# Kernel optimization log

Hardware: AMD Instinct MI355X
Metric: run time of the kernel (lower is better)

## Reference

```python
import jax, jax.numpy as jnp
import numpy as np
import math

C = 1024
CH = C // 2


def setup_inputs() -> dict:
    key = jax.random.key(0)
    ks = jax.random.split(key, 8)
    B, Nq, Nk = 8, 2048, 2048
    y = jax.random.normal(ks[0], (B, Nq, C), dtype=jnp.float32)
    x = jax.random.normal(ks[1], (B, Nk, C), dtype=jnp.float32)
    # torch nn.Linear weights are [out, in]; custom normal init per module
    Wq = jax.random.normal(ks[2], (CH, C), dtype=jnp.float32) * math.sqrt(2.0 / CH)
    Wk = jax.random.normal(ks[3], (CH, C), dtype=jnp.float32) * math.sqrt(2.0 / CH)
    Wv = jax.random.normal(ks[4], (C, C), dtype=jnp.float32) * math.sqrt(2.0 / C)
    # biases keep default torch Linear init: U(-1/sqrt(in), 1/sqrt(in))
    b = 1.0 / math.sqrt(C)
    bq = jax.random.uniform(ks[5], (CH,), minval=-b, maxval=b, dtype=jnp.float32)
    bk = jax.random.uniform(ks[6], (CH,), minval=-b, maxval=b, dtype=jnp.float32)
    bv = jax.random.uniform(ks[7], (C,), minval=-b, maxval=b, dtype=jnp.float32)
    return {"y": y, "x": x, "Wq": Wq, "bq": bq, "Wk": Wk, "bk": bk, "Wv": Wv, "bv": bv}


def reference(y, x, Wq, bq, Wk, bk, Wv, bv):
    scale = (C // 2) ** (-0.5)
    q = jnp.einsum('bnc,hc->bnh', y, Wq) + bq          # [B, Nq, C/2]
    k = jnp.einsum('bmc,hc->bmh', x, Wk) + bk          # [B, Nk, C/2]
    v = jnp.einsum('bmc,dc->bmd', x, Wv) + bv          # [B, Nk, C]
    dots = jnp.einsum('bnh,bmh->bnm', q, k) * scale    # [B, Nq, Nk]
    attn = jax.nn.softmax(dots, axis=-2)               # softmax over QUERY dim
    out = jnp.einsum('bnm,bmd->bnd', attn, v)          # [B, Nq, C]
    return out
```

## Files before the change

kernel.cpp:

```cpp
#include <hip/hip_runtime.h>
#include <hip/hip_bf16.h>


using bf16 = __bf16;
typedef __attribute__((ext_vector_type(8))) __bf16 bf16x8;
typedef __attribute__((ext_vector_type(4))) float f32x4;

#define GLB_AS __attribute__((address_space(1)))
#define LDS_AS __attribute__((address_space(3)))

__device__ __forceinline__ void gload_lds16(const void* g, void* l) {
  __builtin_amdgcn_global_load_lds((const GLB_AS uint32_t*)g,
                                   (LDS_AS uint32_t*)l, 16, 0, 0);
}

#define BAR() __builtin_amdgcn_s_barrier()
#define LGK0() asm volatile("s_waitcnt lgkmcnt(0)" ::: "memory")
#define VM4() asm volatile("s_waitcnt vmcnt(4)" ::: "memory")
#define VM0() asm volatile("s_waitcnt vmcnt(0)" ::: "memory")

enum { EPI_BIAS = 0, EPI_EXP = 1, EPI_OUT = 2 };

template <int EPI>
__global__ __launch_bounds__(512, 2) void gemm256(
    const bf16* __restrict__ A, const bf16* __restrict__ Bt,
    void* __restrict__ Cv, const float* __restrict__ bias,
    float* __restrict__ Z, int M, int N, int K, int ldA, int ldB, int ldC,
    long sA, long sB, long sC, float scale) {
  __shared__ __align__(16) bf16 As[3 * 8192];
  __shared__ __align__(16) bf16 Bs[3 * 8192];

  const int bz = blockIdx.z;
  const bf16* Ab = A + (long)bz * sA;
  const bf16* Bb = Bt + (long)bz * sB;

  const int tid = threadIdx.x;
  const int lane = tid & 63;
  const int wave = tid >> 6;
  const int wr = wave >> 2;
  const int wc = wave & 3;
  const int fl = lane & 15;
  const int kg = lane >> 4;
  const long m0 = (long)blockIdx.x * 256;
  const long n0 = (long)blockIdx.y * 256;

  f32x4 acc[8][4] = {};

  const int js = tid ^ ((tid >> 3) & 7);
  const int srow = js >> 2;
  const int scol = (js & 3) * 8;
  const bf16* gAc = Ab + (m0 + srow) * (long)ldA + scol;
  const bf16* gBc = Bb + (n0 + srow) * (long)ldB + scol;
  char* Abase = (char*)As;
  char* Bbase = (char*)Bs;

#define STAGE_A(tt)                                         \
  {                                                         \
    char* _d = Abase + ((tt) % 3) * 16384 + tid * 16;       \
    const bf16* _g = gAc + (long)(tt) * 32;                 \
    gload_lds16(_g, _d);                                    \
    gload_lds16(_g + 128 * (long)ldA, _d + 8192);           \
  }
#define STAGE_B(tt)                                         \
  {                                                         \
    char* _d = Bbase + ((tt) % 3) * 16384 + tid * 16;       \
    const bf16* _g = gBc + (long)(tt) * 32;                 \
    gload_lds16(_g, _d);                                    \
    gload_lds16(_g + 128 * (long)ldB, _d + 8192);           \
  }

  const int swz = (fl >> 1) << 4;
  const int abase = ((wr * 128 + fl) * 64 + kg * 16) ^ swz;
  const int bbase = ((wc * 64 + fl) * 64 + kg * 16) ^ swz;

  const int nt = K >> 5;

  STAGE_A(0) STAGE_B(0) STAGE_A(1) STAGE_B(1)
  VM4();
  BAR();

  for (int t = 0; t < nt; ++t) {
    const char* Asl = Abase + (t % 3) * 16384;
    const char* Bsl = Bbase + (t % 3) * 16384;
    bf16x8 a[8], b0, b1;
#pragma unroll
    for (int mi = 0; mi < 8; mi++)
      a[mi] = *(const bf16x8*)(Asl + abase + mi * 1024);
    b0 = *(const bf16x8*)(Bsl + bbase);
    b1 = *(const bf16x8*)(Bsl + bbase + 1024);
    if (t + 2 < nt) STAGE_A(t + 2);
    BAR();
    LGK0();
    __builtin_amdgcn_s_setprio(1);
#pragma unroll
    for (int mi = 0; mi < 8; mi++) {
      acc[mi][0] = __builtin_amdgcn_mfma_f32_16x16x32_bf16(a[mi], b0, acc[mi][0], 0, 0, 0);
      acc[mi][1] = __builtin_amdgcn_mfma_f32_16x16x32_bf16(a[mi], b1, acc[mi][1], 0, 0, 0);
    }
    __builtin_amdgcn_s_setprio(0);
    BAR();
    b0 = *(const bf16x8*)(Bsl + bbase + 2 * 1024);
    b1 = *(const bf16x8*)(Bsl + bbase + 3 * 1024);
    if (t + 2 < nt) STAGE_B(t + 2);
    BAR();
    LGK0();
    __builtin_amdgcn_s_setprio(1);
#pragma unroll
    for (int mi = 0; mi < 8; mi++) {
      acc[mi][2] = __builtin_amdgcn_mfma_f32_16x16x32_bf16(a[mi], b0, acc[mi][2], 0, 0, 0);
      acc[mi][3] = __builtin_amdgcn_mfma_f32_16x16x32_bf16(a[mi], b1, acc[mi][3], 0, 0, 0);
    }
    __builtin_amdgcn_s_setprio(0);
    if (t + 2 < nt) { VM4(); } else { VM0(); }
    BAR();
  }
#undef STAGE_A
#undef STAGE_B

  if constexpr (EPI == EPI_BIAS) {
    bf16* Cb = (bf16*)Cv + (long)bz * sC;
#pragma unroll
    for (int j = 0; j < 4; j++) {
      const long cc = n0 + wc * 64 + j * 16 + fl;
      const float bc = bias[cc];
#pragma unroll
      for (int mi = 0; mi < 8; mi++)
#pragma unroll
        for (int e = 0; e < 4; e++) {
          const long rr = m0 + wr * 128 + mi * 16 + kg * 4 + e;
          Cb[rr * ldC + cc] = (bf16)(acc[mi][j][e] + bc);
        }
    }
  } else if constexpr (EPI == EPI_EXP) {
    bf16* Cb = (bf16*)Cv + (long)bz * sC;
    float* Zb = Z + (long)bz * N;
#pragma unroll
    for (int j = 0; j < 4; j++) {
      const long cc = n0 + wc * 64 + j * 16 + fl;
      float zp = 0.f;
#pragma unroll
      for (int mi = 0; mi < 8; mi++)
#pragma unroll
        for (int e = 0; e < 4; e++) {
          const long rr = m0 + wr * 128 + mi * 16 + kg * 4 + e;
          const float ex = __expf(acc[mi][j][e] * scale);
          zp += ex;
          Cb[rr * ldC + cc] = (bf16)ex;
        }
      atomicAdd(&Zb[cc], zp);
    }
  } else {
    float* Cb = (float*)Cv + (long)bz * sC;
#pragma unroll
    for (int j = 0; j < 4; j++) {
      const long cc = n0 + wc * 64 + j * 16 + fl;
#pragma unroll
      for (int mi = 0; mi < 8; mi++)
#pragma unroll
        for (int e = 0; e < 4; e++) {
          const long rr = m0 + wr * 128 + mi * 16 + kg * 4 + e;
          Cb[rr * ldC + cc] = acc[mi][j][e];
        }
    }
  }
}

__global__ void cvt_f32_bf16(const float* __restrict__ in,
                             bf16* __restrict__ out, long n4) {
  long i = blockIdx.x * (long)blockDim.x + threadIdx.x;
  const long stride = (long)gridDim.x * blockDim.x;
  for (; i < n4; i += stride) {
    const float4 f = ((const float4*)in)[i];
    union { ushort4 u; bf16 h[4]; } p;
    p.h[0] = (bf16)f.x;
    p.h[1] = (bf16)f.y;
    p.h[2] = (bf16)f.z;
    p.h[3] = (bf16)f.w;
    ((ushort4*)out)[i] = p.u;
  }
}

__global__ __launch_bounds__(256) void transpose_scale(
    const bf16* __restrict__ kv, const float* __restrict__ Z,
    bf16* __restrict__ vt) {
  __shared__ bf16 tile[32][33];
  const int b = blockIdx.z;
  const bf16* vb = kv + (long)b * 2048 * 1536 + 512;
  bf16* vtb = vt + (long)b * 1024 * 2048;
  const float* Zb = Z + b * 2048;
  const int m0 = blockIdx.x * 32, d0 = blockIdx.y * 32;
  const int t = threadIdx.x;
  const int r = t >> 3, c4 = (t & 7) * 4;

  union { ushort4 u; bf16 h[4]; } in;
  in.u = *(const ushort4*)&vb[(long)(m0 + r) * 1536 + d0 + c4];
  tile[r][c4 + 0] = in.h[0];
  tile[r][c4 + 1] = in.h[1];
  tile[r][c4 + 2] = in.h[2];
  tile[r][c4 + 3] = in.h[3];
  __syncthreads();

  union { ushort4 u; bf16 h[4]; } o;
#pragma unroll
  for (int j = 0; j < 4; j++)
    o.h[j] = (bf16)((float)tile[c4 + j][r] / Zb[m0 + c4 + j]);
  *(ushort4*)&vtb[(long)(d0 + r) * 2048 + m0 + c4] = o.u;
}

extern "C" void kernel_launch(void* const* d_in, const int* in_sizes, int n_in,
                              void* d_out, int out_size, void* d_ws,
                              size_t ws_size, hipStream_t stream) {
  const float* y = (const float*)d_in[0];
  const float* x = (const float*)d_in[1];
  const float* Wq = (const float*)d_in[2];
  const float* bq = (const float*)d_in[3];
  const float* Wk = (const float*)d_in[4];
  const float* bk = (const float*)d_in[5];
  const float* Wv = (const float*)d_in[6];
  const float* bv = (const float*)d_in[7];
  float* out = (float*)d_out;

  constexpr long B = 8, Nq = 2048, Nk = 2048, Cd = 1024, CH = 512;
  constexpr long BN = B * Nq;
  const float scale = 0.04419417382415922f;

  char* w = (char*)d_ws;
  auto alloc = [&](size_t bytes) {
    char* p = w;
    w += (bytes + 255) & ~(size_t)255;
    return p;
  };
  bf16* y_bf = (bf16*)alloc(BN * Cd * 2);
  bf16* x_bf = (bf16*)alloc(BN * Cd * 2);
  bf16* Wq_bf = (bf16*)alloc(CH * Cd * 2);
  bf16* Wkv_bf = (bf16*)alloc((CH + Cd) * Cd * 2);
  float* bkv = (float*)alloc((CH + Cd) * 4);
  bf16* q_bf = (bf16*)alloc(BN * CH * 2);
  bf16* kv_bf = (bf16*)alloc(BN * (CH + Cd) * 2);
  bf16* vt_bf = (bf16*)alloc(BN * Cd * 2);
  bf16* P_bf = (bf16*)alloc(B * Nq * Nk * 2);
  float* Zsum = (float*)alloc(B * Nk * 4);
  if ((size_t)(w - (char*)d_ws) > ws_size) return;

  cvt_f32_bf16<<<2048, 256, 0, stream>>>(y, y_bf, BN * Cd / 4);
  cvt_f32_bf16<<<2048, 256, 0, stream>>>(x, x_bf, BN * Cd / 4);
  cvt_f32_bf16<<<512, 256, 0, stream>>>(Wq, Wq_bf, CH * Cd / 4);
  cvt_f32_bf16<<<512, 256, 0, stream>>>(Wk, Wkv_bf, CH * Cd / 4);
  cvt_f32_bf16<<<1024, 256, 0, stream>>>(Wv, Wkv_bf + CH * Cd, Cd * Cd / 4);
  hipMemcpyAsync(bkv, bk, CH * 4, hipMemcpyDeviceToDevice, stream);
  hipMemcpyAsync(bkv + CH, bv, Cd * 4, hipMemcpyDeviceToDevice, stream);

  gemm256<EPI_BIAS><<<dim3(64, 2, 1), 512, 0, stream>>>(
      y_bf, Wq_bf, q_bf, bq, nullptr, BN, CH, Cd, Cd, Cd, CH, 0, 0, 0, 0.f);
  gemm256<EPI_BIAS><<<dim3(64, 6, 1), 512, 0, stream>>>(
      x_bf, Wkv_bf, kv_bf, bkv, nullptr, BN, CH + Cd, Cd, Cd, Cd, CH + Cd,
      0, 0, 0, 0.f);

  hipMemsetAsync(Zsum, 0, B * Nk * 4, stream);
  gemm256<EPI_EXP><<<dim3(8, 8, 8), 512, 0, stream>>>(
      q_bf, kv_bf, P_bf, nullptr, Zsum, Nq, Nk, CH, CH, CH + Cd, Nk,
      Nq * CH, Nk * (CH + Cd), Nq * Nk, scale);

  transpose_scale<<<dim3(64, 32, 8), 256, 0, stream>>>(kv_bf, Zsum, vt_bf);

  gemm256<EPI_OUT><<<dim3(8, 4, 8), 512, 0, stream>>>(
      P_bf, vt_bf, out, nullptr, nullptr, Nq, Cd, Nk, Nk, Nk, Cd,
      Nq * Nk, Cd * Nk, Nq * Cd, 0.f);
}
```

Before: 472.0 us.

## Replace 256x256 triple-buffered GEMM with simpler 128x128 double-buffered kernel

Replaces the 256x256-tile, 512-thread GEMM with a 128x128-tile, 256-thread kernel. The new kernel double-buffers LDS loads instead of triple-buffering and drops the split-phase barrier choreography and setprio hints. Grids grow fourfold, so there are more blocks to fill the CUs and more occupancy per CU. The cost is lower arithmetic intensity per tile, meaning more global and LDS traffic per FLOP, and less overlap of loads with MFMA work.

```diff
diff --git a/kernel.cpp b/kernel.cpp
--- a/kernel.cpp
+++ b/kernel.cpp
@@ -14,21 +14,16 @@
                                    (LDS_AS uint32_t*)l, 16, 0, 0);
 }
 
-#define BAR() __builtin_amdgcn_s_barrier()
-#define LGK0() asm volatile("s_waitcnt lgkmcnt(0)" ::: "memory")
-#define VM4() asm volatile("s_waitcnt vmcnt(4)" ::: "memory")
-#define VM0() asm volatile("s_waitcnt vmcnt(0)" ::: "memory")
-
 enum { EPI_BIAS = 0, EPI_EXP = 1, EPI_OUT = 2 };
 
 template <int EPI>
-__global__ __launch_bounds__(512, 2) void gemm256(
+__global__ __launch_bounds__(256, 4) void gemm128(
     const bf16* __restrict__ A, const bf16* __restrict__ Bt,
     void* __restrict__ Cv, const float* __restrict__ bias,
     float* __restrict__ Z, int M, int N, int K, int ldA, int ldB, int ldC,
     long sA, long sB, long sC, float scale) {
-  __shared__ __align__(16) bf16 As[3 * 8192];
-  __shared__ __align__(16) bf16 Bs[3 * 8192];
+  __shared__ __align__(16) bf16 As[2 * 4096];
+  __shared__ __align__(16) bf16 Bs[2 * 4096];
 
   const int bz = blockIdx.z;
   const bf16* Ab = A + (long)bz * sA;
@@ -37,14 +32,14 @@
   const int tid = threadIdx.x;
   const int lane = tid & 63;
   const int wave = tid >> 6;
-  const int wr = wave >> 2;
-  const int wc = wave & 3;
+  const int wm = (wave >> 1) * 64;
+  const int wn = (wave & 1) * 64;
   const int fl = lane & 15;
   const int kg = lane >> 4;
-  const long m0 = (long)blockIdx.x * 256;
-  const long n0 = (long)blockIdx.y * 256;
-
-  f32x4 acc[8][4] = {};
+  const long m0 = (long)blockIdx.x * 128;
+  const long n0 = (long)blockIdx.y * 128;
+
+  f32x4 acc[4][4] = {};
 
   const int js = tid ^ ((tid >> 3) & 7);
   const int srow = js >> 2;
@@ -54,81 +49,58 @@
   char* Abase = (char*)As;
   char* Bbase = (char*)Bs;
 
-#define STAGE_A(tt)                                         \
-  {                                                         \
-    char* _d = Abase + ((tt) % 3) * 16384 + tid * 16;       \
-    const bf16* _g = gAc + (long)(tt) * 32;                 \
-    gload_lds16(_g, _d);                                    \
-    gload_lds16(_g + 128 * (long)ldA, _d + 8192);           \
-  }
-#define STAGE_B(tt)                                         \
-  {                                                         \
-    char* _d = Bbase + ((tt) % 3) * 16384 + tid * 16;       \
-    const bf16* _g = gBc + (long)(tt) * 32;                 \
-    gload_lds16(_g, _d);                                    \
-    gload_lds16(_g + 128 * (long)ldB, _d + 8192);           \
-  }
-
-  const int swz = (fl >> 1) << 4;
-  const int abase = ((wr * 128 + fl) * 64 + kg * 16) ^ swz;
-  const int bbase = ((wc * 64 + fl) * 64 + kg * 16) ^ swz;
+#define STAGE(tt)                                            \
+  {                                                          \
+    char* _da = Abase + ((tt)&1) * 8192 + tid * 16;          \
+    char* _db = Bbase + ((tt)&1) * 8192 + tid * 16;          \
+    const bf16* _ga = gAc + (long)(tt) * 32;                 \
+    const bf16* _gb = gBc + (long)(tt) * 32;                 \
+    gload_lds16(_ga, _da);                                   \
+    gload_lds16(_ga + 64 * (long)ldA, _da + 4096);           \
+    gload_lds16(_gb, _db);                                   \
+    gload_lds16(_gb + 64 * (long)ldB, _db + 4096);           \
+  }
+
+  const int swz = ((fl >> 1) & 7) << 4;
+  const int abase = ((wm + fl) * 64 + kg * 16) ^ swz;
+  const int bbase = ((wn + fl) * 64 + kg * 16) ^ swz;
 
   const int nt = K >> 5;
 
-  STAGE_A(0) STAGE_B(0) STAGE_A(1) STAGE_B(1)
-  VM4();
-  BAR();
+  STAGE(0)
+  __syncthreads();
 
   for (int t = 0; t < nt; ++t) {
-    const char* Asl = Abase + (t % 3) * 16384;
-    const char* Bsl = Bbase + (t % 3) * 16384;
-    bf16x8 a[8], b0, b1;
-#pragma unroll
-    for (int mi = 0; mi < 8; mi++)
-      a[mi] = *(const bf16x8*)(Asl + abase + mi * 1024);
-    b0 = *(const bf16x8*)(Bsl + bbase);
-    b1 = *(const bf16x8*)(Bsl + bbase + 1024);
-    if (t + 2 < nt) STAGE_A(t + 2);
-    BAR();
-    LGK0();
-    __builtin_amdgcn_s_setprio(1);
-#pragma unroll
-    for (int mi = 0; mi < 8; mi++) {
-      acc[mi][0] = __builtin_amdgcn_mfma_f32_16x16x32_bf16(a[mi], b0, acc[mi][0], 0, 0, 0);
-      acc[mi][1] = __builtin_amdgcn_mfma_f32_16x16x32_bf16(a[mi], b1, acc[mi][1], 0, 0, 0);
-    }
-    __builtin_amdgcn_s_setprio(0);
-    BAR();
-    b0 = *(const bf16x8*)(Bsl + bbase + 2 * 1024);
-    b1 = *(const bf16x8*)(Bsl + bbase + 3 * 1024);
-    if (t + 2 < nt) STAGE_B(t + 2);
-    BAR();
-    LGK0();
-    __builtin_amdgcn_s_setprio(1);
-#pragma unroll
-    for (int mi = 0; mi < 8; mi++) {
-      acc[mi][2] = __builtin_amdgcn_mfma_f32_16x16x32_bf16(a[mi], b0, acc[mi][2], 0, 0, 0);
-      acc[mi][3] = __builtin_amdgcn_mfma_f32_16x16x32_bf16(a[mi], b1, acc[mi][3], 0, 0, 0);
-    }
-    __builtin_amdgcn_s_setprio(0);
-    if (t + 2 < nt) { VM4(); } else { VM0(); }
-    BAR();
-  }
-#undef STAGE_A
-#undef STAGE_B
+    if (t + 1 < nt) STAGE(t + 1);
+    const char* Asl = Abase + (t & 1) * 8192;
+    const char* Bsl = Bbase + (t & 1) * 8192;
+    bf16x8 a[4], b[4];
+#pragma unroll
+    for (int i = 0; i < 4; i++) a[i] = *(const bf16x8*)(Asl + abase + i * 1024);
+#pragma unroll
+    for (int i = 0; i < 4; i++) b[i] = *(const bf16x8*)(Bsl + bbase + i * 1024);
+#pragma unroll
+    for (int i = 0; i < 4; i++)
+#pragma unroll
+      for (int j = 0; j < 4; j++)
+        acc[i][j] = __builtin_amdgcn_mfma_f32_16x16x32_bf16(a[i], b[j],
+                                                            acc[i][j], 0, 0, 0);
+    __syncthreads();
+  }
+#undef STAGE
 
   if constexpr (EPI == EPI_BIAS) {
     bf16* Cb = (bf16*)Cv + (long)bz * sC;
 #pragma unroll
     for (int j = 0; j < 4; j++) {
-      const long cc = n0 + wc * 64 + j * 16 + fl;
+      const long cc = n0 + wn + j * 16 + fl;
       const float bc = bias[cc];
 #pragma unroll
-      for (int mi = 0; mi < 8; mi++)
+      for (int i = 0; i < 4; i++)
 #pragma unroll
         for (int e = 0; e < 4; e++) {
-          const long rr = m0 + wr * 128 + mi * 16 + kg * 4 + e;
-          Cb[rr * ldC + cc] = (bf16)(acc[mi][j][e] + bc);
+          const long rr = m0 + wm + i * 16 + kg * 4 + e;
+          Cb[rr * ldC + cc] = (bf16)(acc[i][j][e] + bc);
         }
     }
   } else if constexpr (EPI == EPI_EXP) {
@@ -136,14 +108,14 @@
     float* Zb = Z + (long)bz * N;
 #pragma unroll
     for (int j = 0; j < 4; j++) {
-      const long cc = n0 + wc * 64 + j * 16 + fl;
+      const long cc = n0 + wn + j * 16 + fl;
       float zp = 0.f;
 #pragma unroll
-      for (int mi = 0; mi < 8; mi++)
+      for (int i = 0; i < 4; i++)
 #pragma unroll
         for (int e = 0; e < 4; e++) {
-          const long rr = m0 + wr * 128 + mi * 16 + kg * 4 + e;
-          const float ex = __expf(acc[mi][j][e] * scale);
+          const long rr = m0 + wm + i * 16 + kg * 4 + e;
+          const float ex = __expf(acc[i][j][e] * scale);
           zp += ex;
           Cb[rr * ldC + cc] = (bf16)ex;
         }
@@ -153,13 +125,13 @@
     float* Cb = (float*)Cv + (long)bz * sC;
 #pragma unroll
     for (int j = 0; j < 4; j++) {
-      const long cc = n0 + wc * 64 + j * 16 + fl;
-#pragma unroll
-      for (int mi = 0; mi < 8; mi++)
+      const long cc = n0 + wn + j * 16 + fl;
+#pragma unroll
+      for (int i = 0; i < 4; i++)
 #pragma unroll
         for (int e = 0; e < 4; e++) {
-          const long rr = m0 + wr * 128 + mi * 16 + kg * 4 + e;
-          Cb[rr * ldC + cc] = acc[mi][j][e];
+          const long rr = m0 + wm + i * 16 + kg * 4 + e;
+          Cb[rr * ldC + cc] = acc[i][j][e];
         }
     }
   }
@@ -250,20 +222,20 @@
   hipMemcpyAsync(bkv, bk, CH * 4, hipMemcpyDeviceToDevice, stream);
   hipMemcpyAsync(bkv + CH, bv, Cd * 4, hipMemcpyDeviceToDevice, stream);
 
-  gemm256<EPI_BIAS><<<dim3(64, 2, 1), 512, 0, stream>>>(
+  gemm128<EPI_BIAS><<<dim3(128, 4, 1), 256, 0, stream>>>(
       y_bf, Wq_bf, q_bf, bq, nullptr, BN, CH, Cd, Cd, Cd, CH, 0, 0, 0, 0.f);
-  gemm256<EPI_BIAS><<<dim3(64, 6, 1), 512, 0, stream>>>(
+  gemm128<EPI_BIAS><<<dim3(128, 12, 1), 256, 0, stream>>>(
       x_bf, Wkv_bf, kv_bf, bkv, nullptr, BN, CH + Cd, Cd, Cd, Cd, CH + Cd,
       0, 0, 0, 0.f);
 
   hipMemsetAsync(Zsum, 0, B * Nk * 4, stream);
-  gemm256<EPI_EXP><<<dim3(8, 8, 8), 512, 0, stream>>>(
+  gemm128<EPI_EXP><<<dim3(16, 16, 8), 256, 0, stream>>>(
       q_bf, kv_bf, P_bf, nullptr, Zsum, Nq, Nk, CH, CH, CH + Cd, Nk,
       Nq * CH, Nk * (CH + Cd), Nq * Nk, scale);
 
   transpose_scale<<<dim3(64, 32, 8), 256, 0, stream>>>(kv_bf, Zsum, vt_bf);
 
-  gemm256<EPI_OUT><<<dim3(8, 4, 8), 512, 0, stream>>>(
+  gemm128<EPI_OUT><<<dim3(16, 8, 8), 256, 0, stream>>>(
       P_bf, vt_bf, out, nullptr, nullptr, Nq, Cd, Nk, Nk, Nk, Cd,
       Nq * Nk, Cd * Nk, Nq * Cd, 0.f);
 }
```

Result: no change. 474.0 us (+0.4%).
